# Kernel tuning notes

Measured on AMD Instinct MI355X. Metric: run time of the kernel, lower is better.

The kernel has to match this reference:

```python
import jax, jax.numpy as jnp
import numpy as np

B, N, C = 1, 512, 128  # batch, seq (pair rows/cols), pair channel dim
EPS = 1e-5
ENDING = False  # 'outgoing' triangle update (ending=False in the torch module)


def layer_norm(x, w, b):
    mu = jnp.mean(x, axis=-1, keepdims=True)
    var = jnp.mean(jnp.square(x - mu), axis=-1, keepdims=True)
    return (x - mu) * jax.lax.rsqrt(var + EPS) * w + b


def setup_inputs() -> dict:
    key = jax.random.key(0)
    ks = jax.random.split(key, 10)
    s = 0.02
    return {
        "x": jax.random.normal(ks[0], (B, N, N, C), dtype=jnp.float32),
        "norm_in_w": jnp.ones((C,), jnp.float32),
        "norm_in_b": jnp.zeros((C,), jnp.float32),
        "g_in_w": jax.random.normal(ks[1], (2 * C, C), jnp.float32) * s,
        "p_in_w": jax.random.normal(ks[2], (2 * C, C), jnp.float32) * s,
        "g_out_w": jax.random.normal(ks[3], (C, C), jnp.float32) * s,
        "norm_out_w": jnp.ones((C,), jnp.float32),
        "norm_out_b": jnp.zeros((C,), jnp.float32),
        "p_out_w": jax.random.normal(ks[4], (C, C), jnp.float32) * s,
    }


def reference(x, norm_in_w, norm_in_b, g_in_w, p_in_w, g_out_w,
              norm_out_w, norm_out_b, p_out_w):
    # LN -> fused g/p/g_out projections (no bias, as in Boltz)
    xn = layer_norm(x, norm_in_w, norm_in_b)                      # [B,N,N,C]
    g_in = jax.nn.sigmoid(jnp.einsum('bijc,dc->bijd', xn, g_in_w))  # [B,N,N,2C]
    p_in = jnp.einsum('bijc,dc->bijd', xn, p_in_w)                  # [B,N,N,2C]
    pg = p_in * g_in                                                # gated projections
    a = pg[..., :C]   # left projection  [B,N,N,C]
    b = pg[..., C:]   # right projection [B,N,N,C]
    if ENDING:
        tri = jnp.einsum('bkic,bkjc->bijc', a, b)  # incoming edges
    else:
        tri = jnp.einsum('bikc,bjkc->bijc', a, b)  # outgoing edges
    out = layer_norm(tri, norm_out_w, norm_out_b)
    out = jnp.einsum('bijc,dc->bijd', out, p_out_w)                 # [B,N,N,C]
    gate = jax.nn.sigmoid(jnp.einsum('bijc,dc->bijd', xn, g_out_w))
    return out * gate
```

## Files before the change

kernel.cpp:

```cpp
#include <hip/hip_runtime.h>

typedef __bf16 bf16;
typedef __bf16 bf16x4 __attribute__((ext_vector_type(4)));
typedef __bf16 bf16x8 __attribute__((ext_vector_type(8)));
typedef float floatx4 __attribute__((ext_vector_type(4)));

#define NN 512
#define CC 128
#define NROW (NN*NN)

__device__ __forceinline__ void async16(void* lds, const void* g) {
    __builtin_amdgcn_global_load_lds((const __attribute__((address_space(1))) void*)g,
                                     (__attribute__((address_space(3))) void*)lds, 16, 0, 0);
}
__device__ __forceinline__ void wait_vm0() {
    asm volatile("s_waitcnt vmcnt(0)" ::: "memory");
}
__device__ __forceinline__ float sigmoidf(float x) {
    return 1.f / (1.f + __expf(-x));
}

__global__ void setup_kernel(const float* __restrict__ nin_w, const float* __restrict__ nin_b,
                             const float* __restrict__ g_in_w, const float* __restrict__ p_in_w,
                             const float* __restrict__ g_out_w,
                             const float* __restrict__ nout_w, const float* __restrict__ nout_b,
                             const float* __restrict__ p_out_w,
                             bf16* __restrict__ Wall, float* __restrict__ T1, float* __restrict__ T2,
                             bf16* __restrict__ Pp, float* __restrict__ S1, float* __restrict__ S2) {
    int r = blockIdx.x * 256 + threadIdx.x;
    if (r < 640) {
        const float* src = (r < 256) ? (g_in_w + r*CC)
                         : (r < 512) ? (p_in_w + (r-256)*CC)
                                     : (g_out_w + (r-512)*CC);
        float t1 = 0.f, t2 = 0.f;
        for (int c = 0; c < CC; ++c) {
            float wv = src[c];
            float wn = nin_w[c];
            float bn = nin_b[c];
            Wall[r*CC + c] = (bf16)(wv * wn);
            t1 += wn * wv;
            t2 += bn * wv;
        }
        T1[r] = t1; T2[r] = t2;
    } else if (r < 768) {
        int d = r - 640;
        const float* src = p_out_w + d*CC;
        float t1 = 0.f, t2 = 0.f;
        for (int c = 0; c < CC; ++c) {
            float wv = src[c];
            float wn = nout_w[c];
            float bn = nout_b[c];
            Pp[d*CC + c] = (bf16)(wv * wn);
            t1 += wn * wv;
            t2 += bn * wv;
        }
        S1[d] = t1; S2[d] = t2;
    }
}

__global__ __launch_bounds__(256) void k1_ln_proj(
        const float* __restrict__ x, const bf16* __restrict__ Wall,
        const float* __restrict__ T1, const float* __restrict__ T2,
        bf16* __restrict__ a_t, bf16* __restrict__ b_t, bf16* __restrict__ gate) {
    __shared__ char  XS[32768];
    __shared__ float MU[64], RS[64];
    __shared__ char  TB[4][640];

    const int t    = threadIdx.x;
    const int w    = t >> 6, lane = t & 63;
    const int col  = lane & 15, quad = lane >> 4;
    const long r0  = (long)blockIdx.x * 64;

    const char* xg = (const char*)(x + r0 * CC);
    for (int q = 0; q < 8; ++q) {
        int L = q*4096 + t*16;
        int s = L >> 13, row = (L >> 7) & 63, p = (L >> 4) & 7;
        int c = p ^ (row & 7);
        async16(XS + L, xg + row*512 + s*128 + c*16);
    }
    wait_vm0();
    __syncthreads();

    {
        int row = t >> 2, part = t & 3;
        float sum = 0.f, ss = 0.f;
        for (int ch = 0; ch < 8; ++ch) {
            int p = (ch + row + part*2) & 7;
            floatx4 v = *(const floatx4*)(XS + part*8192 + row*128 + p*16);
            for (int j = 0; j < 4; ++j) { float f = v[j]; sum += f; ss += f*f; }
        }
        sum += __shfl_xor(sum, 1, 64); ss += __shfl_xor(ss, 1, 64);
        sum += __shfl_xor(sum, 2, 64); ss += __shfl_xor(ss, 2, 64);
        float mu  = sum * (1.f/128.f);
        float var = ss  * (1.f/128.f) - mu*mu;
        float rs  = rsqrtf(var + 1e-5f);
        if (part == 0) { MU[row] = mu; RS[row] = rs; }
    }
    __syncthreads();

    bf16x8 af[4][4];
    for (int mt = 0; mt < 4; ++mt) {
        int row = mt*16 + col;
        for (int s = 0; s < 4; ++s) {
            floatx4 f0 = *(const floatx4*)(XS + s*8192 + row*128 + (((quad*2+0) ^ (row&7))*16));
            floatx4 f1 = *(const floatx4*)(XS + s*8192 + row*128 + (((quad*2+1) ^ (row&7))*16));
            bf16x8 v;
            v[0]=(bf16)f0[0]; v[1]=(bf16)f0[1]; v[2]=(bf16)f0[2]; v[3]=(bf16)f0[3];
            v[4]=(bf16)f1[0]; v[5]=(bf16)f1[1]; v[6]=(bf16)f1[2]; v[7]=(bf16)f1[3];
            af[mt][s] = v;
        }
    }

    for (int jj = 0; jj < 6; ++jj) {
        int job = w + jj*4;
        if (job < 16) {
            bf16x8 bg[4], bp[4];
            for (int s = 0; s < 4; ++s) {
                bg[s] = *(const bf16x8*)(Wall + (      job*16 + col)*CC + s*32 + quad*8);
                bp[s] = *(const bf16x8*)(Wall + (256 + job*16 + col)*CC + s*32 + quad*8);
            }
            int dg = job*16 + col, dp = 256 + job*16 + col;
            float t1g = T1[dg], t2g = T2[dg], t1p = T1[dp], t2p = T2[dp];
            bf16* dst = (job < 8) ? a_t : b_t;
            int cbase = (job < 8 ? job : job - 8) * 16;
            for (int mt = 0; mt < 4; ++mt) {
                floatx4 ag = {0.f,0.f,0.f,0.f}, ap = {0.f,0.f,0.f,0.f};
                for (int s = 0; s < 4; ++s) {
                    ag = __builtin_amdgcn_mfma_f32_16x16x32_bf16(af[mt][s], bg[s], ag, 0, 0, 0);
                    ap = __builtin_amdgcn_mfma_f32_16x16x32_bf16(af[mt][s], bp[s], ap, 0, 0, 0);
                }
                bf16x4 pk;
                for (int reg = 0; reg < 4; ++reg) {
                    int m = mt*16 + quad*4 + reg;
                    float rs = RS[m], mu = MU[m];
                    float g = rs*ag[reg] - rs*mu*t1g + t2g;
                    float p = rs*ap[reg] - rs*mu*t1p + t2p;
                    pk[reg] = (bf16)(p * sigmoidf(g));
                }
                *(bf16x4*)(TB[w] + col*40 + quad*8) = pk;
                bf16x4 rd = *(const bf16x4*)(TB[w] + (lane >> 2)*40 + (lane & 3)*8);
                int  cg = cbase + (lane >> 2);
                long rg = r0 + mt*16 + (lane & 3)*4;
                *(bf16x4*)(dst + (long)cg * NROW + rg) = rd;
            }
        } else {
            int gc = job - 16;
            bf16x8 bgt[4];
            for (int s = 0; s < 4; ++s)
                bgt[s] = *(const bf16x8*)(Wall + (512 + gc*16 + col)*CC + s*32 + quad*8);
            int dd = 512 + gc*16 + col;
            float t1 = T1[dd], t2 = T2[dd];
            for (int mt = 0; mt < 4; ++mt) {
                floatx4 ac = {0.f,0.f,0.f,0.f};
                for (int s = 0; s < 4; ++s)
                    ac = __builtin_amdgcn_mfma_f32_16x16x32_bf16(af[mt][s], bgt[s], ac, 0, 0, 0);
                for (int reg = 0; reg < 4; ++reg) {
                    int m = mt*16 + quad*4 + reg;
                    float rs = RS[m], mu = MU[m];
                    float g = rs*ac[reg] - rs*mu*t1 + t2;
                    gate[(r0 + m)*CC + gc*16 + col] = (bf16)sigmoidf(g);
                }
            }
        }
    }
}

__global__ __launch_bounds__(256) void k2_tri(
        const bf16* __restrict__ a_t, const bf16* __restrict__ b_t, bf16* __restrict__ tri) {
    __shared__ char As[8192], Bs[8192];
    const int t    = threadIdx.x;
    const int w    = t >> 6, lane = t & 63;
    const int col  = lane & 15, quad = lane >> 4;
    const int c    = blockIdx.y;
    const int i0   = (blockIdx.x >> 2) * 128, j0 = (blockIdx.x & 3) * 128;
    const char* Ac = (const char*)(a_t + (long)c * NROW);
    const char* Bc = (const char*)(b_t + (long)c * NROW);
    const int wm = (w >> 1)*64, wn = (w & 1)*64;

    floatx4 acc[4][4];
    for (int mt = 0; mt < 4; ++mt)
        for (int nt = 0; nt < 4; ++nt) { floatx4 z = {0.f,0.f,0.f,0.f}; acc[mt][nt] = z; }

    for (int k0 = 0; k0 < 512; k0 += 32) {
        __syncthreads();
        for (int q = 0; q < 2; ++q) {
            int L = q*4096 + t*16;
            int row = L >> 6, p = (L >> 4) & 3;
            int cl = p ^ ((row >> 2) & 3);
            async16(As + L, Ac + (i0 + row)*1024 + k0*2 + cl*16);
            async16(Bs + L, Bc + (j0 + row)*1024 + k0*2 + cl*16);
        }
        wait_vm0();
        __syncthreads();
        bf16x8 afr[4], bfr[4];
        for (int mt = 0; mt < 4; ++mt) {
            int row = wm + mt*16 + col;
            afr[mt] = *(const bf16x8*)(As + row*64 + ((quad ^ ((row>>2)&3))*16));
        }
        for (int nt = 0; nt < 4; ++nt) {
            int row = wn + nt*16 + col;
            bfr[nt] = *(const bf16x8*)(Bs + row*64 + ((quad ^ ((row>>2)&3))*16));
        }
        for (int mt = 0; mt < 4; ++mt)
            for (int nt = 0; nt < 4; ++nt)
                acc[mt][nt] = __builtin_amdgcn_mfma_f32_16x16x32_bf16(afr[mt], bfr[nt], acc[mt][nt], 0, 0, 0);
    }
    bf16* Tc = tri + (long)c * NROW;
    for (int mt = 0; mt < 4; ++mt)
        for (int nt = 0; nt < 4; ++nt)
            for (int reg = 0; reg < 4; ++reg) {
                int m = i0 + wm + mt*16 + quad*4 + reg;
                int n = j0 + wn + nt*16 + col;
                Tc[m*512 + n] = (bf16)acc[mt][nt][reg];
            }
}

__global__ __launch_bounds__(256) void k3_out(
        const bf16* __restrict__ tri, const bf16* __restrict__ Pp,
        const float* __restrict__ S1, const float* __restrict__ S2,
        const bf16* __restrict__ gate, float* __restrict__ out) {
    __shared__ char  AS[32768];
    __shared__ float MU[128], RS[128];
    const int t    = threadIdx.x;
    const int w    = t >> 6, lane = t & 63;
    const int col  = lane & 15, quad = lane >> 4;
    const long r0  = (long)blockIdx.x * 128;

    {
        int rg = t & 31;
        int cb = t >> 5;
        for (int it = 0; it < 16; ++it) {
            int cch = it*8 + cb;
            bf16x4 v = *(const bf16x4*)(tri + (long)cch * NROW + r0 + rg*4);
            int ch = cch >> 3, kk = cch & 7;
            for (int u = 0; u < 4; ++u) {
                int row = rg*4 + u;
                *(bf16*)(AS + row*256 + ((ch ^ (row & 15)) * 16) + kk*2) = v[u];
            }
        }
    }
    __syncthreads();

    {
        int row = t >> 1, half = t & 1;
        float sum = 0.f, ss = 0.f;
        for (int cc = 0; cc < 8; ++cc) {
            int j = (half*8 + cc + row) & 15;
            bf16x8 v = *(const bf16x8*)(AS + row*256 + j*16);
            for (int jj = 0; jj < 8; ++jj) { float f = (float)v[jj]; sum += f; ss += f*f; }
        }
        sum += __shfl_xor(sum, 1, 64);
        ss  += __shfl_xor(ss, 1, 64);
        float mu  = sum * (1.f/128.f);
        float var = ss  * (1.f/128.f) - mu*mu;
        float rs  = rsqrtf(var + 1e-5f);
        if (half == 0) { MU[row] = mu; RS[row] = rs; }
    }
    __syncthreads();

    const int wm = (w >> 1)*64, wn = (w & 1)*64;
    floatx4 acc[4][4];
    for (int mt = 0; mt < 4; ++mt)
        for (int nt = 0; nt < 4; ++nt) { floatx4 z = {0.f,0.f,0.f,0.f}; acc[mt][nt] = z; }

    for (int s = 0; s < 4; ++s) {
        bf16x8 bfr[4];
        for (int nt = 0; nt < 4; ++nt)
            bfr[nt] = *(const bf16x8*)(Pp + (wn + nt*16 + col)*CC + s*32 + quad*8);
        for (int mt = 0; mt < 4; ++mt) {
            int row = wm + mt*16 + col;
            bf16x8 afr = *(const bf16x8*)(AS + row*256 + (((s*4 + quad) ^ (row & 15)) * 16));
            for (int nt = 0; nt < 4; ++nt)
                acc[mt][nt] = __builtin_amdgcn_mfma_f32_16x16x32_bf16(afr, bfr[nt], acc[mt][nt], 0, 0, 0);
        }
    }

    for (int mt = 0; mt < 4; ++mt)
        for (int nt = 0; nt < 4; ++nt) {
            int n = wn + nt*16 + col;
            float s1 = S1[n], s2 = S2[n];
            for (int reg = 0; reg < 4; ++reg) {
                int m = wm + mt*16 + quad*4 + reg;
                float rs = RS[m], mu = MU[m];
                float v  = rs*acc[mt][nt][reg] - rs*mu*s1 + s2;
                float gt = (float)gate[(r0 + m)*CC + n];
                out[(r0 + m)*CC + n] = v * gt;
            }
        }
}

extern "C" void kernel_launch(void* const* d_in, const int* in_sizes, int n_in,
                              void* d_out, int out_size, void* d_ws, size_t ws_size,
                              hipStream_t stream) {
    const float* x       = (const float*)d_in[0];
    const float* nin_w   = (const float*)d_in[1];
    const float* nin_b   = (const float*)d_in[2];
    const float* g_in_w  = (const float*)d_in[3];
    const float* p_in_w  = (const float*)d_in[4];
    const float* g_out_w = (const float*)d_in[5];
    const float* nout_w  = (const float*)d_in[6];
    const float* nout_b  = (const float*)d_in[7];
    const float* p_out_w = (const float*)d_in[8];

    char* ws = (char*)d_ws;
    bf16*  Wall = (bf16*)(ws);
    float* T1   = (float*)(ws + 163840);
    float* T2   = (float*)(ws + 166400);
    bf16*  Pp   = (bf16*)(ws + 168960);
    float* S1   = (float*)(ws + 201728);
    float* S2   = (float*)(ws + 202240);
    const long BIG = 67108864L;
    bf16* a_t  = (bf16*)(ws + 204800);
    bf16* b_t  = (bf16*)(ws + 204800 + BIG);
    bf16* gate = (bf16*)(ws + 204800 + 2*BIG);
    bf16* tri  = (bf16*)(ws + 204800 + 3*BIG);
    float* outp = (float*)d_out;

    setup_kernel<<<3, 256, 0, stream>>>(nin_w, nin_b, g_in_w, p_in_w, g_out_w,
                                        nout_w, nout_b, p_out_w,
                                        Wall, T1, T2, Pp, S1, S2);
    k1_ln_proj<<<4096, 256, 0, stream>>>(x, Wall, T1, T2, a_t, b_t, gate);
    k2_tri<<<dim3(16, 128), 256, 0, stream>>>(a_t, b_t, tri);
    k3_out<<<2048, 256, 0, stream>>>(tri, Pp, S1, S2, gate, outp);
}
```

Baseline: 577.8 us.

## Enlarge triangle GEMM tiles, widen transposed stores, and repad out-stage LDS layout

The triangle-multiply kernel now computes 256x128 tiles per block, each wave holding 4x8 accumulators, and is launched with half as many blocks to raise operand reuse per LDS load. The LN/projection kernel reuses the input staging buffer for its transpose, buffers all four row tiles, and then writes 16-byte vectors instead of 8-byte ones. The output kernel gathers four channels per thread into a padded LDS layout instead of an XOR swizzle with scalar stores, and sigmoid uses a hardware reciprocal. These changes trade higher register pressure and fewer resident blocks in the GEMM for better reuse and wider memory transactions.

Result: faster. 537.2 us (-7.0%).

```diff
diff --git a/kernel.cpp b/kernel.cpp
--- a/kernel.cpp
+++ b/kernel.cpp
@@ -17,7 +17,7 @@
     asm volatile("s_waitcnt vmcnt(0)" ::: "memory");
 }
 __device__ __forceinline__ float sigmoidf(float x) {
-    return 1.f / (1.f + __expf(-x));
+    return __builtin_amdgcn_rcpf(1.f + __expf(-x));
 }
 
 __global__ void setup_kernel(const float* __restrict__ nin_w, const float* __restrict__ nin_b,
@@ -64,7 +64,6 @@
         bf16* __restrict__ a_t, bf16* __restrict__ b_t, bf16* __restrict__ gate) {
     __shared__ char  XS[32768];
     __shared__ float MU[64], RS[64];
-    __shared__ char  TB[4][640];
 
     const int t    = threadIdx.x;
     const int w    = t >> 6, lane = t & 63;
@@ -110,6 +109,14 @@
             af[mt][s] = v;
         }
     }
+    float muL[4], rsL[4];
+    for (int mt = 0; mt < 4; ++mt) {
+        muL[mt] = MU[mt*16 + quad*4 + 0];
+        rsL[mt] = RS[mt*16 + quad*4 + 0];
+    }
+    (void)muL; (void)rsL;
+    __syncthreads();
+    char* TBw = XS + w*2304;
 
     for (int jj = 0; jj < 6; ++jj) {
         int job = w + jj*4;
@@ -125,11 +132,13 @@
             int cbase = (job < 8 ? job : job - 8) * 16;
             for (int mt = 0; mt < 4; ++mt) {
                 floatx4 ag = {0.f,0.f,0.f,0.f}, ap = {0.f,0.f,0.f,0.f};
+            #pragma unroll
                 for (int s = 0; s < 4; ++s) {
                     ag = __builtin_amdgcn_mfma_f32_16x16x32_bf16(af[mt][s], bg[s], ag, 0, 0, 0);
                     ap = __builtin_amdgcn_mfma_f32_16x16x32_bf16(af[mt][s], bp[s], ap, 0, 0, 0);
                 }
                 bf16x4 pk;
+            #pragma unroll
                 for (int reg = 0; reg < 4; ++reg) {
                     int m = mt*16 + quad*4 + reg;
                     float rs = RS[m], mu = MU[m];
@@ -137,11 +146,16 @@
                     float p = rs*ap[reg] - rs*mu*t1p + t2p;
                     pk[reg] = (bf16)(p * sigmoidf(g));
                 }
-                *(bf16x4*)(TB[w] + col*40 + quad*8) = pk;
-                bf16x4 rd = *(const bf16x4*)(TB[w] + (lane >> 2)*40 + (lane & 3)*8);
-                int  cg = cbase + (lane >> 2);
-                long rg = r0 + mt*16 + (lane & 3)*4;
-                *(bf16x4*)(dst + (long)cg * NROW + rg) = rd;
+                *(bf16x4*)(TBw + col*144 + mt*32 + quad*8) = pk;
+            }
+            {
+                int c  = lane >> 2;
+                int c0 = lane & 3, c1 = (lane & 3) + 4;
+                bf16x8 r0v = *(const bf16x8*)(TBw + c*144 + c0*16);
+                bf16x8 r1v = *(const bf16x8*)(TBw + c*144 + c1*16);
+                bf16* base = dst + (long)(cbase + c) * NROW + r0;
+                *(bf16x8*)(base + c0*8) = r0v;
+                *(bf16x8*)(base + c1*8) = r1v;
             }
         } else {
             int gc = job - 16;
@@ -152,8 +166,10 @@
             float t1 = T1[dd], t2 = T2[dd];
             for (int mt = 0; mt < 4; ++mt) {
                 floatx4 ac = {0.f,0.f,0.f,0.f};
+            #pragma unroll
                 for (int s = 0; s < 4; ++s)
                     ac = __builtin_amdgcn_mfma_f32_16x16x32_bf16(af[mt][s], bgt[s], ac, 0, 0, 0);
+            #pragma unroll
                 for (int reg = 0; reg < 4; ++reg) {
                     int m = mt*16 + quad*4 + reg;
                     float rs = RS[m], mu = MU[m];
@@ -165,52 +181,57 @@
     }
 }
 
-__global__ __launch_bounds__(256) void k2_tri(
+__global__ __launch_bounds__(256, 2) void k2_tri(
         const bf16* __restrict__ a_t, const bf16* __restrict__ b_t, bf16* __restrict__ tri) {
-    __shared__ char As[8192], Bs[8192];
+    __shared__ char As[16384], Bs[8192];
     const int t    = threadIdx.x;
     const int w    = t >> 6, lane = t & 63;
     const int col  = lane & 15, quad = lane >> 4;
     const int c    = blockIdx.y;
-    const int i0   = (blockIdx.x >> 2) * 128, j0 = (blockIdx.x & 3) * 128;
+    const int i0   = (blockIdx.x >> 2) * 256, j0 = (blockIdx.x & 3) * 128;
     const char* Ac = (const char*)(a_t + (long)c * NROW);
     const char* Bc = (const char*)(b_t + (long)c * NROW);
-    const int wm = (w >> 1)*64, wn = (w & 1)*64;
-
-    floatx4 acc[4][4];
+    const int wm = w * 64;
+
+    floatx4 acc[4][8];
     for (int mt = 0; mt < 4; ++mt)
-        for (int nt = 0; nt < 4; ++nt) { floatx4 z = {0.f,0.f,0.f,0.f}; acc[mt][nt] = z; }
+        for (int nt = 0; nt < 8; ++nt) { floatx4 z = {0.f,0.f,0.f,0.f}; acc[mt][nt] = z; }
 
     for (int k0 = 0; k0 < 512; k0 += 32) {
         __syncthreads();
+        for (int q = 0; q < 4; ++q) {
+            int L = q*4096 + t*16;
+            int row = L >> 6, p = (L >> 4) & 3;
+            int cl = p ^ ((row >> 2) & 3);
+            async16(As + L, Ac + (i0 + row)*1024 + k0*2 + cl*16);
+        }
         for (int q = 0; q < 2; ++q) {
             int L = q*4096 + t*16;
             int row = L >> 6, p = (L >> 4) & 3;
             int cl = p ^ ((row >> 2) & 3);
-            async16(As + L, Ac + (i0 + row)*1024 + k0*2 + cl*16);
             async16(Bs + L, Bc + (j0 + row)*1024 + k0*2 + cl*16);
         }
         wait_vm0();
         __syncthreads();
-        bf16x8 afr[4], bfr[4];
+        bf16x8 afr[4], bfr[8];
         for (int mt = 0; mt < 4; ++mt) {
             int row = wm + mt*16 + col;
             afr[mt] = *(const bf16x8*)(As + row*64 + ((quad ^ ((row>>2)&3))*16));
         }
-        for (int nt = 0; nt < 4; ++nt) {
-            int row = wn + nt*16 + col;
+        for (int nt = 0; nt < 8; ++nt) {
+            int row = nt*16 + col;
             bfr[nt] = *(const bf16x8*)(Bs + row*64 + ((quad ^ ((row>>2)&3))*16));
         }
         for (int mt = 0; mt < 4; ++mt)
-            for (int nt = 0; nt < 4; ++nt)
+            for (int nt = 0; nt < 8; ++nt)
                 acc[mt][nt] = __builtin_amdgcn_mfma_f32_16x16x32_bf16(afr[mt], bfr[nt], acc[mt][nt], 0, 0, 0);
     }
     bf16* Tc = tri + (long)c * NROW;
     for (int mt = 0; mt < 4; ++mt)
-        for (int nt = 0; nt < 4; ++nt)
+        for (int nt = 0; nt < 8; ++nt)
             for (int reg = 0; reg < 4; ++reg) {
                 int m = i0 + wm + mt*16 + quad*4 + reg;
-                int n = j0 + wn + nt*16 + col;
+                int n = j0 + nt*16 + col;
                 Tc[m*512 + n] = (bf16)acc[mt][nt][reg];
             }
 }
@@ -219,34 +240,31 @@
         const bf16* __restrict__ tri, const bf16* __restrict__ Pp,
         const float* __restrict__ S1, const float* __restrict__ S2,
         const bf16* __restrict__ gate, float* __restrict__ out) {
-    __shared__ char  AS[32768];
+    __shared__ char  AS[128*272];
     __shared__ float MU[128], RS[128];
     const int t    = threadIdx.x;
     const int w    = t >> 6, lane = t & 63;
     const int col  = lane & 15, quad = lane >> 4;
     const long r0  = (long)blockIdx.x * 128;
 
-    {
-        int rg = t & 31;
-        int cb = t >> 5;
-        for (int it = 0; it < 16; ++it) {
-            int cch = it*8 + cb;
-            bf16x4 v = *(const bf16x4*)(tri + (long)cch * NROW + r0 + rg*4);
-            int ch = cch >> 3, kk = cch & 7;
-            for (int u = 0; u < 4; ++u) {
-                int row = rg*4 + u;
-                *(bf16*)(AS + row*256 + ((ch ^ (row & 15)) * 16) + kk*2) = v[u];
-            }
-        }
+    for (int it = 0; it < 16; ++it) {
+        int rl = (it & 1)*64 + (t & 63);
+        int cq = (it >> 1)*4 + (t >> 6);
+        const bf16* src = tri + (long)(cq*4) * NROW + r0 + rl;
+        bf16x4 v;
+        v[0] = src[0];
+        v[1] = src[NROW];
+        v[2] = src[2*NROW];
+        v[3] = src[3*NROW];
+        *(bf16x4*)(AS + rl*272 + cq*8) = v;
     }
     __syncthreads();
 
     {
         int row = t >> 1, half = t & 1;
         float sum = 0.f, ss = 0.f;
-        for (int cc = 0; cc < 8; ++cc) {
-            int j = (half*8 + cc + row) & 15;
-            bf16x8 v = *(const bf16x8*)(AS + row*256 + j*16);
+        for (int j = 0; j < 8; ++j) {
+            bf16x8 v = *(const bf16x8*)(AS + row*272 + (half*8 + j)*16);
             for (int jj = 0; jj < 8; ++jj) { float f = (float)v[jj]; sum += f; ss += f*f; }
         }
         sum += __shfl_xor(sum, 1, 64);
@@ -269,7 +287,7 @@
             bfr[nt] = *(const bf16x8*)(Pp + (wn + nt*16 + col)*CC + s*32 + quad*8);
         for (int mt = 0; mt < 4; ++mt) {
             int row = wm + mt*16 + col;
-            bf16x8 afr = *(const bf16x8*)(AS + row*256 + (((s*4 + quad) ^ (row & 15)) * 16));
+            bf16x8 afr = *(const bf16x8*)(AS + row*272 + s*64 + quad*16);
             for (int nt = 0; nt < 4; ++nt)
                 acc[mt][nt] = __builtin_amdgcn_mfma_f32_16x16x32_bf16(afr, bfr[nt], acc[mt][nt], 0, 0, 0);
         }
@@ -320,6 +338,6 @@
                                         nout_w, nout_b, p_out_w,
                                         Wall, T1, T2, Pp, S1, S2);
     k1_ln_proj<<<4096, 256, 0, stream>>>(x, Wall, T1, T2, a_t, b_t, gate);
-    k2_tri<<<dim3(16, 128), 256, 0, stream>>>(a_t, b_t, tri);
+    k2_tri<<<dim3(8, 128), 256, 0, stream>>>(a_t, b_t, tri);
     k3_out<<<2048, 256, 0, stream>>>(tri, Pp, S1, S2, gate, outp);
 }
```
